# Kernel tuning notes

Hardware: AMD Instinct MI355X
Metric: run time of the kernel (lower is better)

## Reference

```python
import jax, jax.numpy as jnp
import numpy as np

VOCAB = 50000
EMBED = 256
HIDDEN = 512
H2 = HIDDEN // 2
TAGS = 32
START = 30
STOP = 31
B = 64
S = 512
NEG = -10000.0


def lstm_scan(x_sbe, h0, c0, wih, whh, bih, bhh, mask_sb):
    # x_sbe: [S,B,E]; masked (packed-sequence-equivalent) unidirectional LSTM.
    def step(carry, inp):
        h, c = carry
        xt, mt = inp
        gates = xt @ wih.T + h @ whh.T + (bih + bhh)  # [B,4*H2], gate order i,f,g,o
        i, f, g, o = jnp.split(gates, 4, axis=-1)
        c_new = jax.nn.sigmoid(f) * c + jax.nn.sigmoid(i) * jnp.tanh(g)
        h_new = jax.nn.sigmoid(o) * jnp.tanh(c_new)
        m = mt[:, None]
        return (jnp.where(m, h_new, h), jnp.where(m, c_new, c)), jnp.where(m, h_new, 0.0)
    _, outs = jax.lax.scan(step, (h0, c0), (x_sbe, mask_sb))
    return outs  # [S,B,H2]


def viterbi(feats, lengths, transitions):
    # feats: [B,S,T]; batched Viterbi with length masking (identity backpointers on pads).
    b, s, t = feats.shape
    init = jnp.full((b, t), NEG, feats.dtype).at[:, START].set(0.0)
    mask = jnp.arange(s)[None, :] < lengths[:, None]
    ident = jnp.arange(t)[None, :]

    def step(fv, inp):
        feat, m = inp
        scores = fv[:, None, :] + transitions[None, :, :]  # [B, next, prev]
        bp = jnp.argmax(scores, axis=-1)                   # [B,T]
        best = jnp.max(scores, axis=-1) + feat
        fv_new = jnp.where(m[:, None], best, fv)
        bp = jnp.where(m[:, None], bp, ident)
        return fv_new, bp

    fv, bps = jax.lax.scan(step, init, (feats.transpose(1, 0, 2), mask.T))
    terminal = fv + transitions[STOP][None, :]
    best_last = jnp.argmax(terminal, axis=-1)  # [B]
    path_score = jnp.take_along_axis(terminal, best_last[:, None], axis=1)[:, 0]

    def back(tag, bp):
        prev = jnp.take_along_axis(bp, tag[:, None], axis=1)[:, 0]
        return prev, tag

    _, path = jax.lax.scan(back, best_last, bps, reverse=True)  # path[t] = tag at step t
    return path_score, path.T  # [B], [B,S]


def setup_inputs() -> dict:
    key = jax.random.key(0)
    ks = jax.random.split(key, 18)
    sc_l = 1.0 / np.sqrt(H2)      # torch LSTM init U(-1/sqrt(H2), 1/sqrt(H2))
    sc_h = 1.0 / np.sqrt(HIDDEN)  # torch Linear init
    u = lambda k, sh, sc: jax.random.uniform(k, sh, jnp.float32, -sc, sc)
    inp = {
        'sentences': jax.random.randint(ks[0], (B, S), 0, VOCAB),
        'lengths': jax.random.randint(ks[1], (B,), S // 2, S + 1).astype(jnp.int32),
        'embedding': jax.random.normal(ks[2], (VOCAB, EMBED), jnp.float32),
        'wih_f': u(ks[3], (4 * H2, EMBED), sc_l),
        'whh_f': u(ks[4], (4 * H2, H2), sc_l),
        'bih_f': u(ks[5], (4 * H2,), sc_l),
        'bhh_f': u(ks[6], (4 * H2,), sc_l),
        'wih_b': u(ks[7], (4 * H2, EMBED), sc_l),
        'whh_b': u(ks[8], (4 * H2, H2), sc_l),
        'bih_b': u(ks[9], (4 * H2,), sc_l),
        'bhh_b': u(ks[10], (4 * H2,), sc_l),
        'w_h2t': u(ks[11], (TAGS, HIDDEN), sc_h),
        'b_h2t': u(ks[12], (TAGS,), sc_h),
        'h0': jax.random.normal(ks[14], (2, B, H2), jnp.float32),
        'c0': jax.random.normal(ks[15], (2, B, H2), jnp.float32),
    }
    trans = jax.random.normal(ks[13], (TAGS, TAGS), jnp.float32)
    inp['transitions'] = trans.at[START, :].set(NEG).at[:, STOP].set(NEG)
    return inp


def reference(sentences, lengths, embedding, wih_f, whh_f, bih_f, bhh_f, wih_b, whh_b, bih_b, bhh_b, w_h2t, b_h2t, transitions, h0, c0):
    emb = embedding[sentences]  # [B,S,E]
    pos = jnp.arange(S)[None, :]
    mask = pos < lengths[:, None]  # [B,S]
    # forward direction
    out_f = lstm_scan(emb.transpose(1, 0, 2), h0[0], c0[0], wih_f, whh_f, bih_f, bhh_f, mask.T)
    # backward direction: reverse each sequence within its own length
    rev_idx = jnp.where(mask, lengths[:, None] - 1 - pos, pos)  # involutive on valid region
    emb_rev = jnp.take_along_axis(emb, rev_idx[:, :, None], axis=1)
    out_b_rev = lstm_scan(emb_rev.transpose(1, 0, 2), h0[1], c0[1], wih_b, whh_b, bih_b, bhh_b, mask.T)
    out_b = jnp.take_along_axis(out_b_rev.transpose(1, 0, 2), rev_idx[:, :, None], axis=1)
    lstm_out = jnp.concatenate([out_f.transpose(1, 0, 2), out_b], axis=-1)  # [B,S,HIDDEN]
    feats = lstm_out @ w_h2t.T + b_h2t  # [B,S,TAGS]
    return viterbi(feats, lengths, transitions)
```

## Files before the change

kernel.cpp:

```cpp
#include <hip/hip_runtime.h>
#include <cstdio>
#include <cstdint>

typedef _Float16 h16;
typedef _Float16 half8 __attribute__((ext_vector_type(8)));
typedef _Float16 half4 __attribute__((ext_vector_type(4)));
typedef float floatx4 __attribute__((ext_vector_type(4)));

#define MFMA16(a, b, c) __builtin_amdgcn_mfma_f32_16x16x32_f16((a), (b), (c), 0, 0, 0)

static constexpr int NB = 64;
static constexpr int NS = 512;
static constexpr int NE = 256;
static constexpr int NH2 = 256;
static constexpr int NG = 1024;
static constexpr int TCH = 256;
static constexpr float LOSCL = 4096.0f;
static constexpr float LOINV = 0.000244140625f;

__device__ __forceinline__ float sigm(float x) { return 1.0f / (1.0f + __expf(-x)); }
__device__ __forceinline__ float tanha(float x) { return 1.0f - 2.0f / (1.0f + __expf(2.0f * x)); }

__global__ void k_prologue(const float* __restrict__ emb,
                           const float* __restrict__ wih_f, const float* __restrict__ wih_b,
                           const float* __restrict__ whh_f, const float* __restrict__ whh_b,
                           const float* __restrict__ w_h2t,
                           const float* __restrict__ bih_f, const float* __restrict__ bhh_f,
                           const float* __restrict__ bih_b, const float* __restrict__ bhh_b,
                           const int* __restrict__ sent, const int* __restrict__ lens,
                           h16* __restrict__ emb_hi, h16* __restrict__ emb_lo,
                           h16* __restrict__ wih_hi, h16* __restrict__ wih_lo,
                           h16* __restrict__ whh_hi, h16* __restrict__ whh_lo,
                           h16* __restrict__ wt_hi, h16* __restrict__ wt_lo,
                           float* __restrict__ bias, int* __restrict__ tok,
                           unsigned* __restrict__ ctr) {
  const int bx = blockIdx.x;
  const int tid = threadIdx.x;
  if (bx < 12500) {
    int i = bx * 256 + tid;
    float4 v = ((const float4*)emb)[i];
    float xs[4] = {v.x, v.y, v.z, v.w};
    half4 hv, lv;
#pragma unroll
    for (int k = 0; k < 4; ++k) {
      h16 h = (h16)xs[k];
      hv[k] = h;
      lv[k] = (h16)((xs[k] - (float)h) * LOSCL);
    }
    ((half4*)emb_hi)[i] = hv;
    ((half4*)emb_lo)[i] = lv;
    return;
  }
  if (bx < 13540) {
    int b2 = bx - 12500;
    const float* src;
    h16 *hi, *lo;
    int li;
    if (b2 < 256)       { src = wih_f; hi = wih_hi;          lo = wih_lo;          li = b2; }
    else if (b2 < 512)  { src = wih_b; hi = wih_hi + 262144; lo = wih_lo + 262144; li = b2 - 256; }
    else if (b2 < 768)  { src = whh_f; hi = whh_hi;          lo = whh_lo;          li = b2 - 512; }
    else if (b2 < 1024) { src = whh_b; hi = whh_hi + 262144; lo = whh_lo + 262144; li = b2 - 768; }
    else                { src = w_h2t; hi = wt_hi;           lo = wt_lo;           li = b2 - 1024; }
    int i = li * 256 + tid;
    float4 v = ((const float4*)src)[i];
    float xs[4] = {v.x, v.y, v.z, v.w};
    half4 hv, lv;
#pragma unroll
    for (int k = 0; k < 4; ++k) {
      h16 h = (h16)xs[k];
      hv[k] = h;
      lv[k] = (h16)((xs[k] - (float)h) * LOSCL);
    }
    ((half4*)hi)[i] = hv;
    ((half4*)lo)[i] = lv;
    return;
  }
  int idx = (bx - 13540) * 256 + tid;
  if (idx < 2048) ctr[idx] = 0u;
  if (idx < 2048) {
    const float* a = (idx < 1024) ? bih_f : bih_b;
    const float* b = (idx < 1024) ? bhh_f : bhh_b;
    int j = idx & 1023;
    bias[idx] = a[j] + b[j];
  }
  int q = idx - 2048;
  if (q >= 0 && q < 2 * NB * NS) {
    int d = q >> 15, r = q & 32767;
    int b = r >> 9, t = r & 511;
    int L = lens[b];
    int pos = (d == 0) ? t : ((t < L) ? (L - 1 - t) : t);
    tok[q] = sent[b * NS + pos];
  }
}

__launch_bounds__(512, 2)
__global__ void k_gemm(const h16* __restrict__ emb_hi, const h16* __restrict__ emb_lo,
                       const h16* __restrict__ wih_hi, const h16* __restrict__ wih_lo,
                       const int* __restrict__ tok, float* __restrict__ gates, int t0) {
  __shared__ h16 lA[2][128 * 64];
  __shared__ h16 lB[2][128 * 64];
  __shared__ int stok[128];

  const int bx = blockIdx.x;
  const int mb = bx & 127;
  const int nb = (bx >> 7) & 7;
  const int d = bx >> 10;
  const int tid = threadIdx.x;
  const int lane = tid & 63;
  const int w = tid >> 6;
  const int wmr = w >> 2;
  const int wnc = w & 3;

  if (tid < 128) {
    int row = mb * 128 + tid;
    int b = row & 63, tl = row >> 6;
    stok[tid] = tok[d * 32768 + b * 512 + (t0 + tl)];
  }
  __syncthreads();

  floatx4 accA[4][2], accB[4][2];
#pragma unroll
  for (int i = 0; i < 4; ++i)
#pragma unroll
    for (int j = 0; j < 2; ++j) { accA[i][j] = (floatx4)0.0f; accB[i][j] = (floatx4)0.0f; }

  auto stage = [&](int kc, int buf) {
    int rg = kc >> 2;
    int krb = (kc & 3) * 64;
    const h16* As = (rg == 1) ? emb_lo : emb_hi;
    const h16* Bs = ((rg == 2) ? wih_lo : wih_hi) + (size_t)d * NG * NE;
#pragma unroll
    for (int i = 0; i < 2; ++i) {
      int c = tid + i * 512;
      int row = c >> 3, x = c & 7, y = x ^ (row & 7);
      half8 va = *(const half8*)(As + (size_t)stok[row] * NE + krb + x * 8);
      *(half8*)&lA[buf][row * 64 + y * 8] = va;
    }
#pragma unroll
    for (int i = 0; i < 2; ++i) {
      int c = tid + i * 512;
      int row = c >> 3, x = c & 7, y = x ^ (row & 7);
      half8 vb = *(const half8*)(Bs + (size_t)(nb * 128 + row) * NE + krb + x * 8);
      *(half8*)&lB[buf][row * 64 + y * 8] = vb;
    }
  };

  stage(0, 0);
  int buf = 0;
  for (int kc = 0; kc < 12; ++kc) {
    __syncthreads();
    if (kc + 1 < 12) stage(kc + 1, buf ^ 1);
    int rg = kc >> 2;
#pragma unroll
    for (int ks = 0; ks < 2; ++ks) {
      half8 af[4], bf[2];
#pragma unroll
      for (int mt = 0; mt < 4; ++mt) {
        int r = wmr * 64 + mt * 16 + (lane & 15);
        int ch = ks * 4 + (lane >> 4);
        af[mt] = *(const half8*)&lA[buf][r * 64 + (ch ^ (r & 7)) * 8];
      }
#pragma unroll
      for (int nt = 0; nt < 2; ++nt) {
        int r = wnc * 32 + nt * 16 + (lane & 15);
        int ch = ks * 4 + (lane >> 4);
        bf[nt] = *(const half8*)&lB[buf][r * 64 + (ch ^ (r & 7)) * 8];
      }
      if (rg == 0) {
#pragma unroll
        for (int mt = 0; mt < 4; ++mt)
#pragma unroll
          for (int nt = 0; nt < 2; ++nt)
            accA[mt][nt] = MFMA16(af[mt], bf[nt], accA[mt][nt]);
      } else {
#pragma unroll
        for (int mt = 0; mt < 4; ++mt)
#pragma unroll
          for (int nt = 0; nt < 2; ++nt)
            accB[mt][nt] = MFMA16(af[mt], bf[nt], accB[mt][nt]);
      }
    }
    buf ^= 1;
  }
#pragma unroll
  for (int mt = 0; mt < 4; ++mt)
#pragma unroll
    for (int nt = 0; nt < 2; ++nt) {
      int col = nb * 128 + wnc * 32 + nt * 16 + (lane & 15);
#pragma unroll
      for (int q = 0; q < 4; ++q) {
        int mrow = mb * 128 + wmr * 64 + mt * 16 + (lane >> 4) * 4 + q;
        gates[((size_t)d * (TCH * 64) + mrow) * 1024 + col] =
            accA[mt][nt][q] + LOINV * accB[mt][nt][q];
      }
    }
}

__launch_bounds__(512, 2)
__global__ void k_recur(const h16* __restrict__ whh_hi, const h16* __restrict__ whh_lo,
                        const float* __restrict__ bias, const float* __restrict__ gates,
                        const int* __restrict__ lens, float* __restrict__ hst,
                        float* __restrict__ cst, uint64_t* h_ex, unsigned* ctr,
                        h16* __restrict__ ho_hi, h16* __restrict__ ho_lo,
                        int t0, int t1) {
  __shared__ h16 hAh[16 * 256];
  __shared__ h16 hAl[16 * 256];
  __shared__ float gbuf[2 * 16 * 68];

  const int bid = blockIdx.x;
  const int d = bid >> 6;
  const int q4 = (bid >> 4) & 3;
  const int g = bid & 15;
  const int gamma = d * 4 + q4;
  const int tid = threadIdx.x;
  const int lane = tid & 63;
  const int w = tid >> 6;
  const int wk = w >> 2;
  const int wnc = w & 3;
  const int l15 = lane & 15, l4 = lane >> 4;

  const int j = wnc * 256 + g * 16 + l15;
  half8 bh[4], bl[4];
#pragma unroll
  for (int ks = 0; ks < 4; ++ks) {
    int k = (wk * 4 + ks) * 32 + l4 * 8;
    bh[ks] = *(const half8*)(whh_hi + ((size_t)d * NG + j) * NE + k);
    bl[ks] = *(const half8*)(whh_lo + ((size_t)d * NG + j) * NE + k);
  }
  const float bias_r = bias[d * 1024 + j];

  const int cl = (tid >> 4) & 15;
  const int u = tid & 15;
  const int chain = q4 * 16 + cl;
  const int lenv = lens[chain];
  float creg = 0.0f, hreg = 0.0f;
  if (tid < 256) {
    creg = cst[((size_t)d * NB + chain) * NH2 + g * 16 + u];
    hreg = hst[((size_t)d * NB + chain) * NH2 + g * 16 + u];
  }

  const int cls0 = tid >> 6;
  const int ksb = (tid * 4) & 255;

  auto grpbase = [&](int phys) -> size_t {
    return ((size_t)(d * 4 + phys) * 64 + q4 * 16) * 128;
  };
  unsigned* h32 = (unsigned*)h_ex;

  float gxp[4];
  auto load_gx = [&](int t, float gdst[4]) {
#pragma unroll
    for (int q = 0; q < 4; ++q) {
      int mrl = l4 * 4 + q;
      int chn = q4 * 16 + mrl;
      gdst[q] = gates[((size_t)d * (TCH * 64) + (t - t0) * 64 + chn) * 1024 + j];
    }
  };
  if (wk == 0) load_gx(t0, gxp);

  for (int t = t0; t < t1; ++t) {
    if (t == t0) {
#pragma unroll
      for (int i = 0; i < 2; ++i) {
        int cls = cls0 + i * 8;
        float4 v = *(const float4*)(hst + ((size_t)d * NB + q4 * 16 + cls) * NH2 + ksb);
        float xs[4] = {v.x, v.y, v.z, v.w};
        half4 hv, lv;
#pragma unroll
        for (int k = 0; k < 4; ++k) {
          h16 hh = (h16)xs[k];
          hv[k] = hh;
          lv[k] = (h16)((xs[k] - (float)hh) * LOSCL);
        }
        int ch = ksb >> 3, y = ch ^ (cls & 7);
        int off = cls * 256 + y * 8 + (ksb & 7);
        *(half4*)&hAh[off] = hv;
        *(half4*)&hAl[off] = lv;
      }
    } else {
      const uint64_t* src64 = h_ex + grpbase(t & 3);
      uint64_t va[4];
#pragma unroll
      for (int i = 0; i < 2; ++i) {
        va[2 * i] = __hip_atomic_load(src64 + tid * 2 + i * 1024, __ATOMIC_RELAXED,
                                      __HIP_MEMORY_SCOPE_AGENT);
        va[2 * i + 1] = __hip_atomic_load(src64 + tid * 2 + 1 + i * 1024, __ATOMIC_RELAXED,
                                          __HIP_MEMORY_SCOPE_AGENT);
      }
#pragma unroll
      for (int i = 0; i < 2; ++i) {
        int cls = cls0 + i * 8;
        uint64_t a = va[2 * i], b = va[2 * i + 1];
        unsigned us[4] = {(unsigned)a, (unsigned)(a >> 32), (unsigned)b, (unsigned)(b >> 32)};
        half4 hv, lv;
#pragma unroll
        for (int k = 0; k < 4; ++k) {
          hv[k] = __builtin_bit_cast(h16, (unsigned short)(us[k] & 0xffffu));
          lv[k] = __builtin_bit_cast(h16, (unsigned short)(us[k] >> 16));
        }
        int ch = ksb >> 3, y = ch ^ (cls & 7);
        int off = cls * 256 + y * 8 + (ksb & 7);
        *(half4*)&hAh[off] = hv;
        *(half4*)&hAl[off] = lv;
      }
    }
    __syncthreads();

    floatx4 aA = (floatx4)0.0f;
    floatx4 aB = (floatx4)0.0f;
#pragma unroll
    for (int ks = 0; ks < 4; ++ks) {
      int ch = (wk * 4 + ks) * 4 + l4;
      int off = l15 * 256 + ((ch ^ (l15 & 7)) * 8);
      half8 ah = *(const half8*)&hAh[off];
      half8 al = *(const half8*)&hAl[off];
      aA = MFMA16(ah, bh[ks], aA);
      aB = MFMA16(ah, bl[ks], aB);
      aB = MFMA16(al, bh[ks], aB);
    }
    {
      int jn = wnc * 16 + l15;
#pragma unroll
      for (int q = 0; q < 4; ++q) {
        int mrl = l4 * 4 + q;
        float v = aA[q] + LOINV * aB[q];
        if (wk == 0) v += gxp[q] + bias_r;
        gbuf[(wk * 16 + mrl) * 68 + jn] = v;
      }
    }
    __syncthreads();

    const bool mk = (t < lenv);
    float hw = 0.0f;
    unsigned wd = 0;
    if (tid < 256) {
      float ig = gbuf[cl * 68 + u]        + gbuf[(16 + cl) * 68 + u];
      float fg = gbuf[cl * 68 + 16 + u]   + gbuf[(16 + cl) * 68 + 16 + u];
      float gg = gbuf[cl * 68 + 32 + u]   + gbuf[(16 + cl) * 68 + 32 + u];
      float og = gbuf[cl * 68 + 48 + u]   + gbuf[(16 + cl) * 68 + 48 + u];
      float cn = sigm(fg) * creg + sigm(ig) * tanha(gg);
      float hn = sigm(og) * tanha(cn);
      if (mk) { creg = cn; hreg = hn; }
      hw = mk ? hn : 0.0f;
      h16 ph = (h16)hreg;
      h16 pl = (h16)((hreg - (float)ph) * LOSCL);
      wd = (unsigned)__builtin_bit_cast(unsigned short, ph) |
           ((unsigned)__builtin_bit_cast(unsigned short, pl) << 16);
    }
    if (t < t1 - 1) {
      if (tid < 256) {
        size_t si = (((size_t)(d * 4 + ((t + 1) & 3)) * 64 + chain) * 256) + g * 16 + u;
        __hip_atomic_store(h32 + si, wd, __ATOMIC_RELAXED, __HIP_MEMORY_SCOPE_AGENT);
      }
      __syncthreads();
      if (tid == 0)
        __hip_atomic_store(&ctr[(gamma * 16 + g) * 16], (unsigned)(t + 1), __ATOMIC_RELAXED,
                           __HIP_MEMORY_SCOPE_AGENT);
    }

    if (tid < 256) {
      int pos = (d == 0) ? t : (mk ? (lenv - 1 - t) : t);
      size_t hoff = ((size_t)chain * NS + pos) * 512 + d * 256 + (size_t)(g * 16 + u);
      h16 a = (h16)hw;
      ho_hi[hoff] = a;
      ho_lo[hoff] = (h16)((hw - (float)a) * LOSCL);
    }
    if (wk == 0 && t + 1 < t1) load_gx(t + 1, gxp);

    if (t < t1 - 1) {
      if (tid < 16) {
        unsigned want = (unsigned)(t + 1);
        while (__hip_atomic_load(&ctr[(gamma * 16 + tid) * 16], __ATOMIC_RELAXED,
                                 __HIP_MEMORY_SCOPE_AGENT) < want)
          __builtin_amdgcn_s_sleep(1);
      }
      __syncthreads();
    }
  }

  if (tid < 256) {
    cst[((size_t)d * NB + chain) * NH2 + g * 16 + u] = creg;
    hst[((size_t)d * NB + chain) * NH2 + g * 16 + u] = hreg;
  }
}

__launch_bounds__(512, 2)
__global__ void k_featsg(const h16* __restrict__ A_hi, const h16* __restrict__ A_lo,
                         const h16* __restrict__ wt_hi, const h16* __restrict__ wt_lo,
                         const float* __restrict__ bt, float* __restrict__ feats) {
  __shared__ h16 lA[2][128 * 64];
  __shared__ h16 lB[2][32 * 64];
  const int mb = blockIdx.x;
  const int tid = threadIdx.x, lane = tid & 63, w = tid >> 6;

  floatx4 accA[2], accB[2];
  accA[0] = accA[1] = (floatx4)0.0f;
  accB[0] = accB[1] = (floatx4)0.0f;

  auto stage = [&](int kc, int buf) {
    int rg = kc >> 3;
    int krb = (kc & 7) * 64;
    const h16* As = (rg == 1) ? A_lo : A_hi;
    const h16* Bs = (rg == 2) ? wt_lo : wt_hi;
#pragma unroll
    for (int i = 0; i < 2; ++i) {
      int c = tid + i * 512;
      int row = c >> 3, x = c & 7, y = x ^ (row & 7);
      half8 v = *(const half8*)(As + (size_t)(mb * 128 + row) * 512 + krb + x * 8);
      *(half8*)&lA[buf][row * 64 + y * 8] = v;
    }
    if (tid < 256) {
      int row = tid >> 3, x = tid & 7, y = x ^ (row & 7);
      half8 v = *(const half8*)(Bs + (size_t)row * 512 + krb + x * 8);
      *(half8*)&lB[buf][row * 64 + y * 8] = v;
    }
  };

  stage(0, 0);
  int buf = 0;
  for (int kc = 0; kc < 24; ++kc) {
    __syncthreads();
    if (kc + 1 < 24) stage(kc + 1, buf ^ 1);
    int rg = kc >> 3;
#pragma unroll
    for (int ks = 0; ks < 2; ++ks) {
      int rA = w * 16 + (lane & 15);
      int ch = ks * 4 + (lane >> 4);
      half8 a = *(const half8*)&lA[buf][rA * 64 + (ch ^ (rA & 7)) * 8];
#pragma unroll
      for (int nt = 0; nt < 2; ++nt) {
        int rB = nt * 16 + (lane & 15);
        half8 b = *(const half8*)&lB[buf][rB * 64 + (ch ^ (rB & 7)) * 8];
        if (rg == 0) accA[nt] = MFMA16(a, b, accA[nt]);
        else         accB[nt] = MFMA16(a, b, accB[nt]);
      }
    }
    buf ^= 1;
  }
#pragma unroll
  for (int nt = 0; nt < 2; ++nt) {
    int col = nt * 16 + (lane & 15);
    float bv = bt[col];
#pragma unroll
    for (int q = 0; q < 4; ++q) {
      int mr = mb * 128 + w * 16 + (lane >> 4) * 4 + q;
      feats[(size_t)mr * 32 + col] = accA[nt][q] + LOINV * accB[nt][q] + bv;
    }
  }
}

__global__ void k_viterbi(const float* __restrict__ feats, const int* __restrict__ lens,
                          const float* __restrict__ trans, float* __restrict__ out) {
  __shared__ float TL[32 * 33];
  __shared__ float fv[2][32];
  __shared__ unsigned char bp[512][32];
  __shared__ unsigned char pth[512];
  __shared__ float sc_sh;

  const int b = blockIdx.x;
  const int tid = threadIdx.x;
  const int L = lens[b];
  const int j = tid & 31, hfx = tid >> 5;

  for (int i = tid; i < 1024; i += 64) {
    int ii = i >> 5, jj = i & 31;
    TL[ii * 33 + jj] = trans[jj * 32 + ii];
  }
  if (tid < 32) fv[0][tid] = (tid == 30) ? 0.0f : -10000.0f;
  __syncthreads();

  const float* fb = feats + (size_t)b * 512 * 32;
  float ftn = fb[j];
  for (int t = 0; t < L; ++t) {
    float ft = ftn;
    if (t + 1 < L) ftn = fb[(t + 1) * 32 + j];
    const float* fcur = fv[t & 1];
    int i0 = hfx * 16;
    float best = fcur[i0] + TL[i0 * 33 + j];
    int bi = i0;
#pragma unroll
    for (int ii = 1; ii < 16; ++ii) {
      int i = i0 + ii;
      float v = fcur[i] + TL[i * 33 + j];
      if (v > best) { best = v; bi = i; }
    }
    float ob = __shfl_xor(best, 32);
    int obi = __shfl_xor(bi, 32);
    if (hfx == 0) {
      if (ob > best) { best = ob; bi = obi; }
      bp[t][j] = (unsigned char)bi;
      fv[(t + 1) & 1][j] = best + ft;
    }
    __syncthreads();
  }
  if (tid == 0) {
    const float* fvf = fv[L & 1];
    float bsc = fvf[0] + TL[0 * 33 + 31];
    int bl = 0;
    for (int i = 1; i < 32; ++i) {
      float v = fvf[i] + TL[i * 33 + 31];
      if (v > bsc) { bsc = v; bl = i; }
    }
    sc_sh = bsc;
    int tag = bl;
    for (int t = 511; t >= 0; --t) {
      pth[t] = (unsigned char)tag;
      if (t < L) tag = bp[t][tag];
    }
  }
  __syncthreads();
  for (int t = tid; t < 512; t += 64) out[64 + (size_t)b * 512 + t] = (float)pth[t];
  if (tid == 0) out[b] = sc_sh;
}

extern "C" void kernel_launch(void* const* d_in, const int* in_sizes, int n_in,
                              void* d_out, int out_size, void* d_ws, size_t ws_size,
                              hipStream_t stream) {
  (void)in_sizes; (void)n_in; (void)out_size;
  const int* sent = (const int*)d_in[0];
  const int* lens = (const int*)d_in[1];
  const float* emb = (const float*)d_in[2];
  const float* wih_f = (const float*)d_in[3];
  const float* whh_f = (const float*)d_in[4];
  const float* bih_f = (const float*)d_in[5];
  const float* bhh_f = (const float*)d_in[6];
  const float* wih_b = (const float*)d_in[7];
  const float* whh_b = (const float*)d_in[8];
  const float* bih_b = (const float*)d_in[9];
  const float* bhh_b = (const float*)d_in[10];
  const float* w_h2t = (const float*)d_in[11];
  const float* b_h2t = (const float*)d_in[12];
  const float* h0 = (const float*)d_in[13];
  const float* c0 = (const float*)d_in[14];
  const float* trans = (const float*)d_in[15];
  float* out = (float*)d_out;

  char* base = (char*)d_ws;
  size_t off = 0;
  auto alloc = [&](size_t bytes) -> void* {
    void* r = base + off;
    off = (off + bytes + 255) & ~(size_t)255;
    return r;
  };
  h16* emb_hi = (h16*)alloc(50000 * 256 * 2);
  h16* emb_lo = (h16*)alloc(50000 * 256 * 2);
  h16* wih_hi = (h16*)alloc(2 * 1024 * 256 * 2);
  h16* wih_lo = (h16*)alloc(2 * 1024 * 256 * 2);
  h16* whh_hi = (h16*)alloc(2 * 1024 * 256 * 2);
  h16* whh_lo = (h16*)alloc(2 * 1024 * 256 * 2);
  h16* wt_hi = (h16*)alloc(32 * 512 * 2);
  h16* wt_lo = (h16*)alloc(32 * 512 * 2);
  float* bias = (float*)alloc(2 * 1024 * 4);
  int* tok = (int*)alloc(2 * 64 * 512 * 4);
  uint64_t* h_ex = (uint64_t*)alloc(2 * 4 * 64 * 256 * 4);
  unsigned* ctr = (unsigned*)alloc(2048 * 4);
  float* hst = (float*)alloc(2 * 64 * 256 * 4);
  float* cst = (float*)alloc(2 * 64 * 256 * 4);
  float* feats = (float*)alloc((size_t)64 * 512 * 32 * 4);
  h16* ho_hi = (h16*)alloc((size_t)64 * 512 * 512 * 2);
  h16* ho_lo = (h16*)alloc((size_t)64 * 512 * 512 * 2);
  float* gates = (float*)alloc((size_t)2 * TCH * 64 * 1024 * 4);

  if (off > ws_size) {
    fprintf(stderr, "kernel_launch: need %zu ws bytes, have %zu\n", off, ws_size);
    return;
  }

  k_prologue<<<13804, 256, 0, stream>>>(emb, wih_f, wih_b, whh_f, whh_b, w_h2t,
                                        bih_f, bhh_f, bih_b, bhh_b, sent, lens,
                                        emb_hi, emb_lo, wih_hi, wih_lo, whh_hi, whh_lo,
                                        wt_hi, wt_lo, bias, tok, ctr);
  hipMemcpyAsync(hst, h0, 2 * 64 * 256 * 4, hipMemcpyDeviceToDevice, stream);
  hipMemcpyAsync(cst, c0, 2 * 64 * 256 * 4, hipMemcpyDeviceToDevice, stream);

  for (int chunk = 0; chunk < 2; ++chunk) {
    int t0 = chunk * TCH, t1 = t0 + TCH;
    k_gemm<<<2048, 512, 0, stream>>>(emb_hi, emb_lo, wih_hi, wih_lo, tok, gates, t0);
    k_recur<<<128, 512, 0, stream>>>(whh_hi, whh_lo, bias, gates, lens, hst, cst, h_ex,
                                     ctr, ho_hi, ho_lo, t0, t1);
  }
  k_featsg<<<256, 512, 0, stream>>>(ho_hi, ho_lo, wt_hi, wt_lo, b_h2t, feats);
  k_viterbi<<<64, 64, 0, stream>>>(feats, lens, trans, out);
}
```

Before: 1.534 ms.

## Split LSTM recurrence into 8-chain batch groups across 256 blocks

The persistent recurrence kernel now assigns 8 batch chains per block group instead of 16, doubling the grid to 256 blocks and the number of synchronization counters. Each block loads half as much exchanged hidden state per step and runs half as many elementwise gate threads, aiming to shorten the per-timestep critical path and spread the work over more compute units. In exchange, the 16-row MFMA tiles now carry duplicated rows, so half the matrix work is wasted. The recurrent weights are also read by twice as many blocks, and more blocks take part in the inter-block spin-wait handshakes.

```diff
diff --git a/kernel.cpp b/kernel.cpp
--- a/kernel.cpp
+++ b/kernel.cpp
@@ -76,7 +76,7 @@
     return;
   }
   int idx = (bx - 13540) * 256 + tid;
-  if (idx < 2048) ctr[idx] = 0u;
+  if (idx < 4096) ctr[idx] = 0u;
   if (idx < 2048) {
     const float* a = (idx < 1024) ? bih_f : bih_b;
     const float* b = (idx < 1024) ? bhh_f : bhh_b;
@@ -203,15 +203,15 @@
                         float* __restrict__ cst, uint64_t* h_ex, unsigned* ctr,
                         h16* __restrict__ ho_hi, h16* __restrict__ ho_lo,
                         int t0, int t1) {
-  __shared__ h16 hAh[16 * 256];
-  __shared__ h16 hAl[16 * 256];
-  __shared__ float gbuf[2 * 16 * 68];
+  __shared__ h16 hAh[8 * 256];
+  __shared__ h16 hAl[8 * 256];
+  __shared__ float gbuf[2 * 8 * 68];
 
   const int bid = blockIdx.x;
-  const int d = bid >> 6;
-  const int q4 = (bid >> 4) & 3;
+  const int d = bid >> 7;
+  const int q8 = (bid >> 4) & 7;
   const int g = bid & 15;
-  const int gamma = d * 4 + q4;
+  const int gamma = d * 8 + q8;
   const int tid = threadIdx.x;
   const int lane = tid & 63;
   const int w = tid >> 6;
@@ -229,12 +229,12 @@
   }
   const float bias_r = bias[d * 1024 + j];
 
-  const int cl = (tid >> 4) & 15;
+  const int cl = (tid >> 4) & 7;
   const int u = tid & 15;
-  const int chain = q4 * 16 + cl;
+  const int chain = q8 * 8 + cl;
   const int lenv = lens[chain];
   float creg = 0.0f, hreg = 0.0f;
-  if (tid < 256) {
+  if (tid < 128) {
     creg = cst[((size_t)d * NB + chain) * NH2 + g * 16 + u];
     hreg = hst[((size_t)d * NB + chain) * NH2 + g * 16 + u];
   }
@@ -243,7 +243,7 @@
   const int ksb = (tid * 4) & 255;
 
   auto grpbase = [&](int phys) -> size_t {
-    return ((size_t)(d * 4 + phys) * 64 + q4 * 16) * 128;
+    return ((size_t)(d * 4 + phys) * 64 + q8 * 8) * 128;
   };
   unsigned* h32 = (unsigned*)h_ex;
 
@@ -252,80 +252,68 @@
 #pragma unroll
     for (int q = 0; q < 4; ++q) {
       int mrl = l4 * 4 + q;
-      int chn = q4 * 16 + mrl;
+      int chn = q8 * 8 + mrl;
       gdst[q] = gates[((size_t)d * (TCH * 64) + (t - t0) * 64 + chn) * 1024 + j];
     }
   };
-  if (wk == 0) load_gx(t0, gxp);
+  if (wk == 0 && l4 < 2) load_gx(t0, gxp);
 
   for (int t = t0; t < t1; ++t) {
     if (t == t0) {
-#pragma unroll
-      for (int i = 0; i < 2; ++i) {
-        int cls = cls0 + i * 8;
-        float4 v = *(const float4*)(hst + ((size_t)d * NB + q4 * 16 + cls) * NH2 + ksb);
-        float xs[4] = {v.x, v.y, v.z, v.w};
-        half4 hv, lv;
-#pragma unroll
-        for (int k = 0; k < 4; ++k) {
-          h16 hh = (h16)xs[k];
-          hv[k] = hh;
-          lv[k] = (h16)((xs[k] - (float)hh) * LOSCL);
-        }
-        int ch = ksb >> 3, y = ch ^ (cls & 7);
-        int off = cls * 256 + y * 8 + (ksb & 7);
-        *(half4*)&hAh[off] = hv;
-        *(half4*)&hAl[off] = lv;
-      }
+      float4 v = *(const float4*)(hst + ((size_t)d * NB + q8 * 8 + cls0) * NH2 + ksb);
+      float xs[4] = {v.x, v.y, v.z, v.w};
+      half4 hv, lv;
+#pragma unroll
+      for (int k = 0; k < 4; ++k) {
+        h16 hh = (h16)xs[k];
+        hv[k] = hh;
+        lv[k] = (h16)((xs[k] - (float)hh) * LOSCL);
+      }
+      int ch = ksb >> 3, y = ch ^ (cls0 & 7);
+      int off = cls0 * 256 + y * 8 + (ksb & 7);
+      *(half4*)&hAh[off] = hv;
+      *(half4*)&hAl[off] = lv;
     } else {
       const uint64_t* src64 = h_ex + grpbase(t & 3);
-      uint64_t va[4];
-#pragma unroll
-      for (int i = 0; i < 2; ++i) {
-        va[2 * i] = __hip_atomic_load(src64 + tid * 2 + i * 1024, __ATOMIC_RELAXED,
-                                      __HIP_MEMORY_SCOPE_AGENT);
-        va[2 * i + 1] = __hip_atomic_load(src64 + tid * 2 + 1 + i * 1024, __ATOMIC_RELAXED,
-                                          __HIP_MEMORY_SCOPE_AGENT);
-      }
-#pragma unroll
-      for (int i = 0; i < 2; ++i) {
-        int cls = cls0 + i * 8;
-        uint64_t a = va[2 * i], b = va[2 * i + 1];
-        unsigned us[4] = {(unsigned)a, (unsigned)(a >> 32), (unsigned)b, (unsigned)(b >> 32)};
-        half4 hv, lv;
-#pragma unroll
-        for (int k = 0; k < 4; ++k) {
-          hv[k] = __builtin_bit_cast(h16, (unsigned short)(us[k] & 0xffffu));
-          lv[k] = __builtin_bit_cast(h16, (unsigned short)(us[k] >> 16));
-        }
-        int ch = ksb >> 3, y = ch ^ (cls & 7);
-        int off = cls * 256 + y * 8 + (ksb & 7);
-        *(half4*)&hAh[off] = hv;
-        *(half4*)&hAl[off] = lv;
-      }
+      uint64_t a = __hip_atomic_load(src64 + tid * 2, __ATOMIC_RELAXED,
+                                     __HIP_MEMORY_SCOPE_AGENT);
+      uint64_t b = __hip_atomic_load(src64 + tid * 2 + 1, __ATOMIC_RELAXED,
+                                     __HIP_MEMORY_SCOPE_AGENT);
+      unsigned us[4] = {(unsigned)a, (unsigned)(a >> 32), (unsigned)b, (unsigned)(b >> 32)};
+      half4 hv, lv;
+#pragma unroll
+      for (int k = 0; k < 4; ++k) {
+        hv[k] = __builtin_bit_cast(h16, (unsigned short)(us[k] & 0xffffu));
+        lv[k] = __builtin_bit_cast(h16, (unsigned short)(us[k] >> 16));
+      }
+      int ch = ksb >> 3, y = ch ^ (cls0 & 7);
+      int off = cls0 * 256 + y * 8 + (ksb & 7);
+      *(half4*)&hAh[off] = hv;
+      *(half4*)&hAl[off] = lv;
     }
     __syncthreads();
 
     floatx4 aA = (floatx4)0.0f;
     floatx4 aB = (floatx4)0.0f;
+    const int br = l15 & 7;
 #pragma unroll
     for (int ks = 0; ks < 4; ++ks) {
       int ch = (wk * 4 + ks) * 4 + l4;
-      int off = l15 * 256 + ((ch ^ (l15 & 7)) * 8);
+      int off = br * 256 + ((ch ^ br) * 8);
       half8 ah = *(const half8*)&hAh[off];
       half8 al = *(const half8*)&hAl[off];
       aA = MFMA16(ah, bh[ks], aA);
       aB = MFMA16(ah, bl[ks], aB);
       aB = MFMA16(al, bh[ks], aB);
     }
-    {
+    if (l4 < 2) {
       int jn = wnc * 16 + l15;
 #pragma unroll
       for (int q = 0; q < 4; ++q) {
         int mrl = l4 * 4 + q;
         float v = aA[q] + LOINV * aB[q];
         if (wk == 0) v += gxp[q] + bias_r;
-        gbuf[(wk * 16 + mrl) * 68 + jn] = v;
+        gbuf[(wk * 8 + mrl) * 68 + jn] = v;
       }
     }
     __syncthreads();
@@ -333,11 +321,11 @@
     const bool mk = (t < lenv);
     float hw = 0.0f;
     unsigned wd = 0;
-    if (tid < 256) {
-      float ig = gbuf[cl * 68 + u]        + gbuf[(16 + cl) * 68 + u];
-      float fg = gbuf[cl * 68 + 16 + u]   + gbuf[(16 + cl) * 68 + 16 + u];
-      float gg = gbuf[cl * 68 + 32 + u]   + gbuf[(16 + cl) * 68 + 32 + u];
-      float og = gbuf[cl * 68 + 48 + u]   + gbuf[(16 + cl) * 68 + 48 + u];
+    if (tid < 128) {
+      float ig = gbuf[cl * 68 + u]      + gbuf[(8 + cl) * 68 + u];
+      float fg = gbuf[cl * 68 + 16 + u] + gbuf[(8 + cl) * 68 + 16 + u];
+      float gg = gbuf[cl * 68 + 32 + u] + gbuf[(8 + cl) * 68 + 32 + u];
+      float og = gbuf[cl * 68 + 48 + u] + gbuf[(8 + cl) * 68 + 48 + u];
       float cn = sigm(fg) * creg + sigm(ig) * tanha(gg);
       float hn = sigm(og) * tanha(cn);
       if (mk) { creg = cn; hreg = hn; }
@@ -348,7 +336,7 @@
            ((unsigned)__builtin_bit_cast(unsigned short, pl) << 16);
     }
     if (t < t1 - 1) {
-      if (tid < 256) {
+      if (tid < 128) {
         size_t si = (((size_t)(d * 4 + ((t + 1) & 3)) * 64 + chain) * 256) + g * 16 + u;
         __hip_atomic_store(h32 + si, wd, __ATOMIC_RELAXED, __HIP_MEMORY_SCOPE_AGENT);
       }
@@ -358,14 +346,14 @@
                            __HIP_MEMORY_SCOPE_AGENT);
     }
 
-    if (tid < 256) {
+    if (tid < 128) {
       int pos = (d == 0) ? t : (mk ? (lenv - 1 - t) : t);
       size_t hoff = ((size_t)chain * NS + pos) * 512 + d * 256 + (size_t)(g * 16 + u);
       h16 a = (h16)hw;
       ho_hi[hoff] = a;
       ho_lo[hoff] = (h16)((hw - (float)a) * LOSCL);
     }
-    if (wk == 0 && t + 1 < t1) load_gx(t + 1, gxp);
+    if (wk == 0 && l4 < 2 && t + 1 < t1) load_gx(t + 1, gxp);
 
     if (t < t1 - 1) {
       if (tid < 16) {
@@ -378,7 +366,7 @@
     }
   }
 
-  if (tid < 256) {
+  if (tid < 128) {
     cst[((size_t)d * NB + chain) * NH2 + g * 16 + u] = creg;
     hst[((size_t)d * NB + chain) * NH2 + g * 16 + u] = hreg;
   }
@@ -553,7 +541,7 @@
   float* bias = (float*)alloc(2 * 1024 * 4);
   int* tok = (int*)alloc(2 * 64 * 512 * 4);
   uint64_t* h_ex = (uint64_t*)alloc(2 * 4 * 64 * 256 * 4);
-  unsigned* ctr = (unsigned*)alloc(2048 * 4);
+  unsigned* ctr = (unsigned*)alloc(4096 * 4);
   float* hst = (float*)alloc(2 * 64 * 256 * 4);
   float* cst = (float*)alloc(2 * 64 * 256 * 4);
   float* feats = (float*)alloc((size_t)64 * 512 * 32 * 4);
@@ -576,7 +564,7 @@
   for (int chunk = 0; chunk < 2; ++chunk) {
     int t0 = chunk * TCH, t1 = t0 + TCH;
     k_gemm<<<2048, 512, 0, stream>>>(emb_hi, emb_lo, wih_hi, wih_lo, tok, gates, t0);
-    k_recur<<<128, 512, 0, stream>>>(whh_hi, whh_lo, bias, gates, lens, hst, cst, h_ex,
+    k_recur<<<256, 512, 0, stream>>>(whh_hi, whh_lo, bias, gates, lens, hst, cst, h_ex,
                                      ctr, ho_hi, ho_lo, t0, t1);
   }
   k_featsg<<<256, 512, 0, stream>>>(ho_hi, ho_lo, wt_hi, wt_lo, b_h2t, feats);
```

After: 1.478 ms. 1.04x faster.
